# Kernel optimization log

Measured on AMD Instinct MI355X. Metric: run time of the kernel, lower is better.

The kernel has to match this reference:

```python
import jax, jax.numpy as jnp
import numpy as np

PRE_NMS_LIMIT = 6000
PROPOSAL_COUNT = 1000
NMS_THRESHOLD = 0.7
RPN_BBOX_STD_DEV = np.array([0.1, 0.1, 0.2, 0.2], dtype=np.float32)
NEG_INF = -1e30


def setup_inputs() -> dict:
    key = jax.random.key(0)
    k1, k2, k3 = jax.random.split(key, 3)
    B, N = 8, 262144
    rpn_probs = jax.random.uniform(k1, (B, N, 2), dtype=jnp.float32)
    rpn_bbox = jax.random.normal(k2, (B, N, 4), dtype=jnp.float32)
    anchors = jax.random.uniform(k3, (B, N, 4), dtype=jnp.float32)
    return {"rpn_probs": rpn_probs, "rpn_bbox": rpn_bbox, "anchors": anchors}


def apply_box_deltas(boxes, deltas):
    # boxes: [..., (y1,x1,y2,x2)], deltas: [..., (dy,dx,log(dh),log(dw))]
    h = boxes[..., 2] - boxes[..., 0]
    w = boxes[..., 3] - boxes[..., 1]
    cy = boxes[..., 0] + 0.5 * h
    cx = boxes[..., 1] + 0.5 * w
    cy = cy + deltas[..., 0] * h
    cx = cx + deltas[..., 1] * w
    h = h * jnp.exp(deltas[..., 2])
    w = w * jnp.exp(deltas[..., 3])
    y1 = cy - 0.5 * h
    x1 = cx - 0.5 * w
    return jnp.stack([y1, x1, y1 + h, x1 + w], axis=-1)


def clip_boxes(boxes):
    # window = [0, 0, 1, 1]
    return jnp.clip(boxes, 0.0, 1.0)


def nms_single(boxes, scores, max_out, iou_thresh):
    # Greedy NMS on one image. boxes [K,4] (sorted by score desc), scores [K].
    y1, x1, y2, x2 = boxes[:, 0], boxes[:, 1], boxes[:, 2], boxes[:, 3]
    areas = (y2 - y1) * (x2 - x1)

    def step(s, _):
        i = jnp.argmax(s)
        valid = s[i] > NEG_INF
        by1, bx1, by2, bx2 = y1[i], x1[i], y2[i], x2[i]
        iy1 = jnp.maximum(y1, by1)
        ix1 = jnp.maximum(x1, bx1)
        iy2 = jnp.minimum(y2, by2)
        ix2 = jnp.minimum(x2, bx2)
        inter = jnp.maximum(iy2 - iy1, 0.0) * jnp.maximum(ix2 - ix1, 0.0)
        union = areas + areas[i] - inter
        iou = inter / jnp.maximum(union, 1e-12)
        suppress = iou > iou_thresh
        s = jnp.where(suppress, NEG_INF, s)
        s = s.at[i].set(NEG_INF)
        return s, (i, valid)

    s0 = jnp.where(jnp.isfinite(scores), scores, NEG_INF)
    _, (idx, valid) = jax.lax.scan(step, s0, None, length=max_out)
    return idx, valid


def reference(rpn_probs, rpn_bbox, anchors):
    scores = rpn_probs[:, :, 1]                               # [B, N]
    deltas = rpn_bbox * RPN_BBOX_STD_DEV.reshape(1, 1, 4)     # [B, N, 4]

    pre_nms = min(PRE_NMS_LIMIT, anchors.shape[1])
    top_scores, ix = jax.lax.top_k(scores, pre_nms)           # [B, K], [B, K]
    deltas = jnp.take_along_axis(deltas, ix[:, :, None], axis=1)
    pre_nms_anchors = jnp.take_along_axis(anchors, ix[:, :, None], axis=1)

    boxes = clip_boxes(apply_box_deltas(pre_nms_anchors, deltas))  # [B, K, 4]

    idx, valid = jax.vmap(lambda b, s: nms_single(b, s, PROPOSAL_COUNT, NMS_THRESHOLD))(boxes, top_scores)
    sel = jnp.take_along_axis(boxes, idx[:, :, None], axis=1)      # [B, P, 4]
    proposals = jnp.where(valid[:, :, None], sel, 0.0)             # pad invalid with zeros
    return proposals
```

## Files before the change

kernel.cpp:

```cpp
#include <hip/hip_runtime.h>
#include <stdint.h>

#define NB 8
#define NN 262144
#define KTOP 6000
#define CAP 8192
#define NOUT 1000
#define IOU_THR 0.7f
#define NGROUPS ((KTOP + 63) / 64)
#define NF4B (NN * 2 / 4)

#define OFF_HIST 0
#define OFF_CNT  32768
#define OFF_CUT  33792
#define OFF_KEYS 34048
#define OFF_SIDX 558336
#define OFF_CBOX 750336
#define OFF_CAR  1518336

__device__ __forceinline__ int binOf(unsigned int u) {
  if (u & 0x80000000u) return 0;
  if (u >= 0x3F000000u) {
    unsigned int r = 512u + ((u - 0x3F000000u) >> 14);
    return (int)(r > 1023u ? 1023u : r);
  }
  return (int)(u >> 23);
}

__global__ void k0_init(unsigned int* __restrict__ hist, unsigned int* __restrict__ cnt,
                        unsigned long long* __restrict__ keys) {
  int i = blockIdx.x * blockDim.x + threadIdx.x;
  if (i < NB * CAP) keys[i] = ~0ull;
  if (i < NB * 1024) hist[i] = 0u;
  if (i < NB * 32) cnt[i] = 0u;
}

__global__ __launch_bounds__(256) void k1_hist(const float4* __restrict__ probs4,
                                               unsigned int* __restrict__ hist) {
  __shared__ unsigned int lh[1024];
  int t = threadIdx.x;
  for (int i = t; i < 1024; i += 256) lh[i] = 0u;
  __syncthreads();
  int b = blockIdx.x >> 5;
  int blk = blockIdx.x & 31;
  size_t base = (size_t)b * NF4B + (size_t)blk * 4096;
#pragma unroll 4
  for (int it = 0; it < 16; ++it) {
    float4 f = probs4[base + it * 256 + t];
    atomicAdd(&lh[binOf(__float_as_uint(f.y))], 1u);
    atomicAdd(&lh[binOf(__float_as_uint(f.w))], 1u);
  }
  __syncthreads();
  for (int i = t; i < 1024; i += 256)
    if (lh[i]) atomicAdd(&hist[b * 1024 + i], lh[i]);
}

__global__ void k2_cut(const unsigned int* __restrict__ hist, int* __restrict__ cut) {
  int w = threadIdx.x >> 6, lane = threadIdx.x & 63;
  if (w >= NB) return;
  unsigned int carry = 0; int cb = 0; bool found = false;
  for (int c = 0; c < 16 && !found; ++c) {
    int bin = 1023 - c * 64 - lane;
    unsigned int v = hist[w * 1024 + bin];
    unsigned int p = v;
    for (int d = 1; d < 64; d <<= 1) {
      unsigned int q = __shfl_up(p, d);
      if (lane >= d) p += q;
    }
    unsigned int cum = carry + p;
    unsigned long long m = __ballot(cum >= KTOP);
    if (m) { int fl = __builtin_ctzll(m); cb = 1023 - c * 64 - fl; found = true; }
    carry += __shfl(p, 63);
  }
  if (lane == 0) cut[w] = cb;
}

__global__ __launch_bounds__(256) void k3_compact(const float4* __restrict__ probs4,
                                                  const int* __restrict__ cut,
                                                  unsigned int* __restrict__ cnt,
                                                  unsigned long long* __restrict__ keys) {
  __shared__ unsigned int waveSums[4];
  __shared__ unsigned int blockBase;
  int t = threadIdx.x, lane = t & 63, w = t >> 6;
  int b = blockIdx.x >> 5;
  int blk = blockIdx.x & 31;
  int cb = cut[b];
  size_t base = (size_t)b * NF4B + (size_t)blk * 4096;
  unsigned int mask = 0;
#pragma unroll 4
  for (int it = 0; it < 16; ++it) {
    float4 f = probs4[base + it * 256 + t];
    if (binOf(__float_as_uint(f.y)) >= cb) mask |= 1u << (2 * it);
    if (binOf(__float_as_uint(f.w)) >= cb) mask |= 1u << (2 * it + 1);
  }
  unsigned int cntT = __popc(mask);
  unsigned int pre = cntT;
  for (int d = 1; d < 64; d <<= 1) {
    unsigned int q = __shfl_up(pre, d);
    if (lane >= d) pre += q;
  }
  if (lane == 63) waveSums[w] = pre;
  __syncthreads();
  if (t == 0) {
    unsigned int tot = waveSums[0] + waveSums[1] + waveSums[2] + waveSums[3];
    blockBase = atomicAdd(&cnt[b * 32], tot);
  }
  __syncthreads();
  unsigned int mybase = blockBase + (pre - cntT);
  for (int m = 0; m < w; ++m) mybase += waveSums[m];
  if (mask) {
    unsigned int kk = 0;
    for (int it = 0; it < 16; ++it) {
      if (mask & (3u << (2 * it))) {
        float4 f = probs4[base + it * 256 + t];
        unsigned int e0 = ((unsigned int)(blk * 4096 + it * 256 + t)) * 2;
        if (mask & (1u << (2 * it))) {
          unsigned int pos = mybase + kk++;
          if (pos < CAP)
            keys[(size_t)b * CAP + pos] =
                ((unsigned long long)(~__float_as_uint(f.y)) << 32) | e0;
        }
        if (mask & (1u << (2 * it + 1))) {
          unsigned int pos = mybase + kk++;
          if (pos < CAP)
            keys[(size_t)b * CAP + pos] =
                ((unsigned long long)(~__float_as_uint(f.w)) << 32) | (e0 + 1);
        }
      }
    }
  }
}


__global__ __launch_bounds__(128) void k4a_sortchunk(unsigned long long* __restrict__ keys) {
  __shared__ unsigned long long sk[1024];
  int b = blockIdx.x >> 3, c = blockIdx.x & 7;
  int t = threadIdx.x;
  size_t gb = (size_t)b * CAP + (size_t)c * 1024;
  int gl = c * 1024 + 8 * t;
  unsigned long long v[8];
#pragma unroll
  for (int r = 0; r < 8; ++r) v[r] = keys[gb + 8 * t + r];
#pragma unroll
  for (int kk = 2; kk <= 8; kk <<= 1) {
#pragma unroll
    for (int j = kk >> 1; j >= 1; j >>= 1) {
#pragma unroll
      for (int r = 0; r < 8; ++r) {
        if ((r & j) == 0) {
          bool up = (((gl + r) & kk) == 0);
          unsigned long long a = v[r], bb = v[r | j];
          if ((a > bb) == up) { v[r] = bb; v[r | j] = a; }
        }
      }
    }
  }
  for (int kk = 16; kk <= 1024; kk <<= 1) {
    bool up = ((gl & kk) == 0);
    for (int j = kk >> 1; j >= 8; j >>= 1) {
#pragma unroll
      for (int r = 0; r < 8; ++r) sk[r * 128 + t] = v[r];
      __syncthreads();
      int p = t ^ (j >> 3);
      bool lower = ((t & (j >> 3)) == 0);
      bool wmin = (lower == up);
#pragma unroll
      for (int r = 0; r < 8; ++r) {
        unsigned long long pv = sk[r * 128 + p];
        bool gt = v[r] > pv;
        v[r] = (gt == wmin) ? pv : v[r];
      }
      __syncthreads();
    }
#pragma unroll
    for (int j = 4; j >= 1; j >>= 1)
#pragma unroll
      for (int r = 0; r < 8; ++r)
        if ((r & j) == 0) {
          unsigned long long a = v[r], bb = v[r | j];
          if ((a > bb) == up) { v[r] = bb; v[r | j] = a; }
        }
  }
#pragma unroll
  for (int r = 0; r < 8; ++r) keys[gb + 8 * t + r] = v[r];
}

template <int KK>
__global__ __launch_bounds__(KK / 8) void k4_phase(unsigned long long* __restrict__ keys,
                                                   unsigned int* __restrict__ sortedIdx) {
  __shared__ unsigned long long sk[KK];
  constexpr int NT = KK / 8;
  constexpr int NCH = CAP / KK;
  int b = blockIdx.x / NCH, c = blockIdx.x % NCH;
  int t = threadIdx.x;
  size_t gb = (size_t)b * CAP + (size_t)c * KK;
  int gl = c * KK + 8 * t;
  unsigned long long v[8];
#pragma unroll
  for (int r = 0; r < 8; ++r) v[r] = keys[gb + 8 * t + r];
  bool up = ((gl & KK) == 0);
  for (int j = KK >> 1; j >= 8; j >>= 1) {
#pragma unroll
    for (int r = 0; r < 8; ++r) sk[r * NT + t] = v[r];
    __syncthreads();
    int p = t ^ (j >> 3);
    bool lower = ((t & (j >> 3)) == 0);
    bool wmin = (lower == up);
#pragma unroll
    for (int r = 0; r < 8; ++r) {
      unsigned long long pv = sk[r * NT + p];
      bool gt = v[r] > pv;
      v[r] = (gt == wmin) ? pv : v[r];
    }
    __syncthreads();
  }
#pragma unroll
  for (int j = 4; j >= 1; j >>= 1)
#pragma unroll
    for (int r = 0; r < 8; ++r)
      if ((r & j) == 0) {
        unsigned long long a = v[r], bb = v[r | j];
        if ((a > bb) == up) { v[r] = bb; v[r | j] = a; }
      }
  if (KK == CAP) {
#pragma unroll
    for (int r = 0; r < 8; ++r) {
      int gi = gl + r;
      if (gi < KTOP) sortedIdx[b * KTOP + gi] = (unsigned int)(v[r] & 0xFFFFFFFFull);
    }
  } else {
#pragma unroll
    for (int r = 0; r < 8; ++r) keys[gb + 8 * t + r] = v[r];
  }
}

__global__ void k5_boxes(const unsigned int* __restrict__ sortedIdx,
                         const float4* __restrict__ anchors, const float4* __restrict__ bbox,
                         float4* __restrict__ cbox, float* __restrict__ car) {
  int tid = blockIdx.x * blockDim.x + threadIdx.x;
  if (tid >= NB * KTOP) return;
  int b = tid / KTOP;
  unsigned int idx = sortedIdx[tid];
  float4 a = anchors[(size_t)b * NN + idx];
  float4 d = bbox[(size_t)b * NN + idx];
  {
#pragma clang fp contract(off)
    float dy = d.x * 0.1f, dx = d.y * 0.1f, dh = d.z * 0.2f, dw = d.w * 0.2f;
    float h = a.z - a.x;
    float w = a.w - a.y;
    float cy = a.x + 0.5f * h;
    float cx = a.y + 0.5f * w;
    cy = cy + dy * h;
    cx = cx + dx * w;
    h = h * expf(dh);
    w = w * expf(dw);
    float y1 = cy - 0.5f * h;
    float x1 = cx - 0.5f * w;
    float y2 = y1 + h;
    float x2 = x1 + w;
    y1 = fminf(fmaxf(y1, 0.0f), 1.0f);
    x1 = fminf(fmaxf(x1, 0.0f), 1.0f);
    y2 = fminf(fmaxf(y2, 0.0f), 1.0f);
    x2 = fminf(fmaxf(x2, 0.0f), 1.0f);
    float4 o; o.x = y1; o.y = x1; o.z = y2; o.w = x2;
    cbox[tid] = o;
    car[tid] = (y2 - y1) * (x2 - x1);
  }
}

__device__ __forceinline__ bool iouSup(float y1, float x1, float y2, float x2, float ar,
                                       float by1, float bx1, float by2, float bx2, float bar) {
#pragma clang fp contract(off)
  float iy1 = fmaxf(y1, by1);
  float ix1 = fmaxf(x1, bx1);
  float iy2 = fminf(y2, by2);
  float ix2 = fminf(x2, bx2);
  float inter = fmaxf(iy2 - iy1, 0.0f) * fmaxf(ix2 - ix1, 0.0f);
  float uni = (ar + bar) - inter;
  float iou = inter / fmaxf(uni, 1e-12f);
  return iou > IOU_THR;
}

__global__ __launch_bounds__(1024) void k6_nms(const float4* __restrict__ cbox,
                                               const float* __restrict__ car,
                                               float* __restrict__ out) {
  __shared__ float sy1[1088], sx1[1088], sy2[1088], sx2[1088], sar[1088];
  __shared__ float g_y1[2][64], g_x1[2][64], g_y2[2][64], g_x2[2][64], g_ar[2][64];
  __shared__ unsigned long long rowMat[64];
  __shared__ unsigned long long preSuppPart[16];
  __shared__ int nselSh, nsuppSh;
  int b = blockIdx.x, t = threadIdx.x;
  int lane = t & 63, w = t >> 6;

  if (t < 64) {
    if (t < KTOP) {
      float4 bx = cbox[(size_t)b * KTOP + t];
      g_y1[0][t] = bx.x; g_x1[0][t] = bx.y; g_y2[0][t] = bx.z; g_x2[0][t] = bx.w;
      g_ar[0][t] = car[(size_t)b * KTOP + t];
    }
  }
  if (t == 0) { nselSh = 0; nsuppSh = 0; }
  __syncthreads();

  for (int g = 0; g < NGROUPS; ++g) {
    int p = g & 1;
    int gs = g * 64;
    int validCnt = (KTOP - gs < 64) ? (KTOP - gs) : 64;

    if (w == 15 && g + 1 < NGROUPS) {
      int idx2 = gs + 64 + lane;
      if (idx2 < KTOP) {
        float4 bx = cbox[(size_t)b * KTOP + idx2];
        int q = p ^ 1;
        g_y1[q][lane] = bx.x; g_x1[q][lane] = bx.y;
        g_y2[q][lane] = bx.z; g_x2[q][lane] = bx.w;
        g_ar[q][lane] = car[(size_t)b * KTOP + idx2];
      }
    }
    float cy1 = g_y1[p][lane], cx1 = g_x1[p][lane];
    float cy2 = g_y2[p][lane], cx2 = g_x2[p][lane], ca = g_ar[p][lane];
    bool cpos = (cy2 > cy1) && (cx2 > cx1);

    {
      int nsupp = nsuppSh;
      bool s = false;
      if (cpos) {
        for (int si = w; si < nsupp; si += 16) {
          if (iouSup(cy1, cx1, cy2, cx2, ca,
                     sy1[si], sx1[si], sy2[si], sx2[si], sar[si])) { s = true; break; }
        }
      }
      unsigned long long m = __ballot(s);
      if (lane == 0) preSuppPart[w] = m;
    }
#pragma unroll
    for (int r = 0; r < 4; ++r) {
      int i = w * 4 + r;
      float by1 = g_y1[p][i], bx1 = g_x1[p][i];
      float by2 = g_y2[p][i], bx2 = g_x2[p][i], bar = g_ar[p][i];
      unsigned long long rowm = 0ull;
      if ((by2 > by1) && (bx2 > bx1)) {
        bool kill = iouSup(cy1, cx1, cy2, cx2, ca, by1, bx1, by2, bx2, bar);
        rowm = __ballot(kill);
      }
      if (lane == 0) rowMat[i] = rowm;
    }
    __syncthreads();

    if (t < 64) {
      int nsel0 = nselSh, nsupp0 = nsuppSh;
      unsigned long long rr = rowMat[t];
      unsigned int rLo = (unsigned int)rr, rHi = (unsigned int)(rr >> 32);
      unsigned long long preSupp = 0ull;
#pragma unroll
      for (int c2 = 0; c2 < 16; ++c2) preSupp |= preSuppPart[c2];
      unsigned long long validMask =
          (validCnt >= 64) ? ~0ull : ((1ull << validCnt) - 1ull);
      unsigned long long posMask = __ballot(cpos);
      unsigned long long alive = validMask & ~preSupp;
      unsigned long long selm = alive & ~posMask;
      unsigned long long work = alive & posMask;
      while (work) {
        int jj = __builtin_ctzll(work);
        selm |= (1ull << jj);
        unsigned int lo = (unsigned int)__builtin_amdgcn_readlane((int)rLo, jj);
        unsigned int hi = (unsigned int)__builtin_amdgcn_readlane((int)rHi, jj);
        work &= ~(((unsigned long long)hi << 32) | lo);
        work &= ~(1ull << jj);
      }
      bool sel = ((selm >> t) & 1ull) != 0ull;
      if (sel) {
        int rank = nsel0 + (int)__popcll(selm & ((1ull << t) - 1ull));
        if (rank < NOUT) {
          float4 o; o.x = cy1; o.y = cx1; o.z = cy2; o.w = cx2;
          ((float4*)out)[(size_t)b * NOUT + rank] = o;
        }
      }
      bool canSup = sel && cpos;
      unsigned long long csm = __ballot(canSup);
      if (canSup) {
        int rs = nsupp0 + (int)__popcll(csm & ((1ull << t) - 1ull));
        sy1[rs] = cy1; sx1[rs] = cx1; sy2[rs] = cy2; sx2[rs] = cx2; sar[rs] = ca;
      }
      if (t == 0) {
        nselSh = nsel0 + (int)__popcll(selm);
        nsuppSh = nsupp0 + (int)__popcll(csm);
      }
    }
    __syncthreads();
    if (nselSh >= NOUT) break;
  }

  __syncthreads();
  int nf = nselSh < NOUT ? nselSh : NOUT;
  for (int k2 = nf * 4 + t; k2 < NOUT * 4; k2 += 1024)
    out[(size_t)b * NOUT * 4 + k2] = 0.0f;
}

extern "C" void kernel_launch(void* const* d_in, const int* in_sizes, int n_in,
                              void* d_out, int out_size, void* d_ws, size_t ws_size,
                              hipStream_t stream) {
  (void)in_sizes; (void)n_in; (void)out_size; (void)ws_size;
  const float* probs = (const float*)d_in[0];
  const float4* bbox = (const float4*)d_in[1];
  const float4* anchors = (const float4*)d_in[2];
  float* out = (float*)d_out;
  char* ws = (char*)d_ws;

  unsigned int* hist = (unsigned int*)(ws + OFF_HIST);
  unsigned int* cnt = (unsigned int*)(ws + OFF_CNT);
  int* cut = (int*)(ws + OFF_CUT);
  unsigned long long* keys = (unsigned long long*)(ws + OFF_KEYS);
  unsigned int* sidx = (unsigned int*)(ws + OFF_SIDX);
  float4* cbox = (float4*)(ws + OFF_CBOX);
  float* car = (float*)(ws + OFF_CAR);

  k0_init<<<256, 256, 0, stream>>>(hist, cnt, keys);
  k1_hist<<<256, 256, 0, stream>>>((const float4*)probs, hist);
  k2_cut<<<1, 512, 0, stream>>>(hist, cut);
  k3_compact<<<256, 256, 0, stream>>>((const float4*)probs, cut, cnt, keys);
  k4a_sortchunk<<<NB * 8, 128, 0, stream>>>(keys);
  k4_phase<2048><<<NB * 4, 256, 0, stream>>>(keys, sidx);
  k4_phase<4096><<<NB * 2, 512, 0, stream>>>(keys, sidx);
  k4_phase<8192><<<NB, 1024, 0, stream>>>(keys, sidx);
  k5_boxes<<<(NB * KTOP + 255) / 256, 256, 0, stream>>>(sidx, anchors, bbox, cbox, car);
  k6_nms<<<NB, 1024, 0, stream>>>(cbox, car, out);
}
```

Before: 222.7 us.

## Compact positive-area boxes before NMS and emit zero-area selections separately

A scan kernel compacts boxes with positive area into a slot list, so the serial NMS loop iterates only over boxes that can suppress or be suppressed. Zero-area boxes, which are always selected and never suppress, get their output ranks afterwards in an emit kernel using per-group selection bitmasks and prefix counts. NMS also stops early once the remaining zero-area boxes would fill the output. The histogram kernel is simplified to merge low-value bins into a single counter, which reduces shared-memory atomics. This adds two kernel launches and extra workspace traffic.

```diff
diff --git a/kernel.cpp b/kernel.cpp
--- a/kernel.cpp
+++ b/kernel.cpp
@@ -7,8 +7,8 @@
 #define CAP 8192
 #define NOUT 1000
 #define IOU_THR 0.7f
-#define NGROUPS ((KTOP + 63) / 64)
 #define NF4B (NN * 2 / 4)
+#define PPAD 6016
 
 #define OFF_HIST 0
 #define OFF_CNT  32768
@@ -17,14 +17,19 @@
 #define OFF_SIDX 558336
 #define OFF_CBOX 750336
 #define OFF_CAR  1518336
-
-__device__ __forceinline__ int binOf(unsigned int u) {
+#define OFF_NPOS (OFF_HIST + 0)
+#define OFF_SELW (OFF_HIST + 1024)
+#define OFF_SELP (OFF_HIST + 7168)
+#define OFF_STOP (OFF_HIST + 10368)
+#define OFF_NVAL (OFF_HIST + 10624)
+#define OFF_PPRE (OFF_KEYS)
+#define OFF_PSLOT (OFF_KEYS + 192512)
+
+__device__ __forceinline__ int binOf2(unsigned int u) {
   if (u & 0x80000000u) return 0;
-  if (u >= 0x3F000000u) {
-    unsigned int r = 512u + ((u - 0x3F000000u) >> 14);
-    return (int)(r > 1023u ? 1023u : r);
-  }
-  return (int)(u >> 23);
+  if (u < 0x3F000000u) return 0;
+  unsigned int r = (u - 0x3F000000u) >> 14;
+  return (int)(512u + (r > 511u ? 511u : r));
 }
 
 __global__ void k0_init(unsigned int* __restrict__ hist, unsigned int* __restrict__ cnt,
@@ -44,12 +49,17 @@
   int b = blockIdx.x >> 5;
   int blk = blockIdx.x & 31;
   size_t base = (size_t)b * NF4B + (size_t)blk * 4096;
+  unsigned int lowCnt = 0;
 #pragma unroll 4
   for (int it = 0; it < 16; ++it) {
     float4 f = probs4[base + it * 256 + t];
-    atomicAdd(&lh[binOf(__float_as_uint(f.y))], 1u);
-    atomicAdd(&lh[binOf(__float_as_uint(f.w))], 1u);
-  }
+    unsigned int u1 = __float_as_uint(f.y), u2 = __float_as_uint(f.w);
+    if ((u1 & 0x80000000u) || u1 < 0x3F000000u) ++lowCnt;
+    else { unsigned int r = (u1 - 0x3F000000u) >> 14; atomicAdd(&lh[512 + (r > 511u ? 511u : r)], 1u); }
+    if ((u2 & 0x80000000u) || u2 < 0x3F000000u) ++lowCnt;
+    else { unsigned int r = (u2 - 0x3F000000u) >> 14; atomicAdd(&lh[512 + (r > 511u ? 511u : r)], 1u); }
+  }
+  if (lowCnt) atomicAdd(&lh[0], lowCnt);
   __syncthreads();
   for (int i = t; i < 1024; i += 256)
     if (lh[i]) atomicAdd(&hist[b * 1024 + i], lh[i]);
@@ -90,8 +100,8 @@
 #pragma unroll 4
   for (int it = 0; it < 16; ++it) {
     float4 f = probs4[base + it * 256 + t];
-    if (binOf(__float_as_uint(f.y)) >= cb) mask |= 1u << (2 * it);
-    if (binOf(__float_as_uint(f.w)) >= cb) mask |= 1u << (2 * it + 1);
+    if (binOf2(__float_as_uint(f.y)) >= cb) mask |= 1u << (2 * it);
+    if (binOf2(__float_as_uint(f.w)) >= cb) mask |= 1u << (2 * it + 1);
   }
   unsigned int cntT = __popc(mask);
   unsigned int pre = cntT;
@@ -130,7 +140,6 @@
     }
   }
 }
-
 
 __global__ __launch_bounds__(128) void k4a_sortchunk(unsigned long long* __restrict__ keys) {
   __shared__ unsigned long long sk[1024];
@@ -268,6 +277,46 @@
   }
 }
 
+__global__ __launch_bounds__(1024) void k5b_scan(const float4* __restrict__ cbox,
+                                                 unsigned int* __restrict__ posPre,
+                                                 unsigned int* __restrict__ pslot,
+                                                 unsigned int* __restrict__ nposArr) {
+  __shared__ unsigned int waveSums[16];
+  __shared__ unsigned int carrySh;
+  int b = blockIdx.x, t = threadIdx.x, lane = t & 63, w = t >> 6;
+  if (t == 0) carrySh = 0;
+  __syncthreads();
+  for (int base = 0; base < KTOP; base += 1024) {
+    int i = base + t;
+    bool pos = false;
+    if (i < KTOP) {
+      float4 bx = cbox[(size_t)b * KTOP + i];
+      pos = (bx.z > bx.x) && (bx.w > bx.y);
+    }
+    unsigned long long m = __ballot(pos);
+    unsigned int pre = (unsigned int)__popcll(m & ((1ull << lane) - 1ull));
+    if (lane == 0) waveSums[w] = (unsigned int)__popcll(m);
+    __syncthreads();
+    unsigned int wbase = 0, total = 0;
+#pragma unroll
+    for (int mm = 0; mm < 16; ++mm) {
+      unsigned int v = waveSums[mm];
+      if (mm < w) wbase += v;
+      total += v;
+    }
+    unsigned int carry = carrySh;
+    if (i < KTOP) {
+      unsigned int excl = carry + wbase + pre;
+      posPre[(size_t)b * PPAD + i] = excl;
+      if (pos) pslot[(size_t)b * PPAD + excl] = (unsigned int)i;
+    }
+    __syncthreads();
+    if (t == 0) carrySh = carry + total;
+  }
+  __syncthreads();
+  if (t == 0) nposArr[b * 32] = carrySh;
+}
+
 __device__ __forceinline__ bool iouSup(float y1, float x1, float y2, float x2, float ar,
                                        float by1, float bx1, float by2, float bx2, float bar) {
 #pragma clang fp contract(off)
@@ -283,51 +332,53 @@
 
 __global__ __launch_bounds__(1024) void k6_nms(const float4* __restrict__ cbox,
                                                const float* __restrict__ car,
-                                               float* __restrict__ out) {
-  __shared__ float sy1[1088], sx1[1088], sy2[1088], sx2[1088], sar[1088];
-  __shared__ float g_y1[2][64], g_x1[2][64], g_y2[2][64], g_x2[2][64], g_ar[2][64];
+                                               const unsigned int* __restrict__ pslot,
+                                               const unsigned int* __restrict__ nposArr,
+                                               unsigned long long* __restrict__ selW,
+                                               unsigned int* __restrict__ selP,
+                                               unsigned int* __restrict__ stopArr,
+                                               unsigned int* __restrict__ nvalArr) {
+  __shared__ float4 selBox[1088];
+  __shared__ float selAr[1088];
+  __shared__ float4 gbox[2][64];
+  __shared__ float gar[2][64];
   __shared__ unsigned long long rowMat[64];
   __shared__ unsigned long long preSuppPart[16];
-  __shared__ int nselSh, nsuppSh;
-  int b = blockIdx.x, t = threadIdx.x;
-  int lane = t & 63, w = t >> 6;
-
-  if (t < 64) {
-    if (t < KTOP) {
-      float4 bx = cbox[(size_t)b * KTOP + t];
-      g_y1[0][t] = bx.x; g_x1[0][t] = bx.y; g_y2[0][t] = bx.z; g_x2[0][t] = bx.w;
-      g_ar[0][t] = car[(size_t)b * KTOP + t];
-    }
-  }
-  if (t == 0) { nselSh = 0; nsuppSh = 0; }
-  __syncthreads();
-
-  for (int g = 0; g < NGROUPS; ++g) {
-    int p = g & 1;
-    int gs = g * 64;
-    int validCnt = (KTOP - gs < 64) ? (KTOP - gs) : 64;
-
-    if (w == 15 && g + 1 < NGROUPS) {
-      int idx2 = gs + 64 + lane;
-      if (idx2 < KTOP) {
-        float4 bx = cbox[(size_t)b * KTOP + idx2];
+  __shared__ int selCntSh, stopSh;
+  int b = blockIdx.x, t = threadIdx.x, lane = t & 63, w = t >> 6;
+  int npos = (int)nposArr[b * 32];
+  int ngroups = (npos + 63) >> 6;
+  const unsigned int* ps = pslot + (size_t)b * PPAD;
+  if (t == 0) { selCntSh = 0; stopSh = 0; }
+  if (t < 64 && t < npos) {
+    unsigned int s0 = ps[t];
+    gbox[0][t] = cbox[(size_t)b * KTOP + s0];
+    gar[0][t] = car[(size_t)b * KTOP + s0];
+  }
+  __syncthreads();
+
+  for (int g = 0; g < ngroups; ++g) {
+    int p = g & 1, j0 = g * 64;
+    int cnt2 = (npos - j0 < 64) ? (npos - j0) : 64;
+    if (w == 15 && g + 1 < ngroups) {
+      int j2 = j0 + 64 + lane;
+      if (j2 < npos) {
+        unsigned int s2 = ps[j2];
         int q = p ^ 1;
-        g_y1[q][lane] = bx.x; g_x1[q][lane] = bx.y;
-        g_y2[q][lane] = bx.z; g_x2[q][lane] = bx.w;
-        g_ar[q][lane] = car[(size_t)b * KTOP + idx2];
-      }
-    }
-    float cy1 = g_y1[p][lane], cx1 = g_x1[p][lane];
-    float cy2 = g_y2[p][lane], cx2 = g_x2[p][lane], ca = g_ar[p][lane];
-    bool cpos = (cy2 > cy1) && (cx2 > cx1);
-
+        gbox[q][lane] = cbox[(size_t)b * KTOP + s2];
+        gar[q][lane] = car[(size_t)b * KTOP + s2];
+      }
+    }
+    float4 cb4 = gbox[p][lane];
+    float ca = gar[p][lane];
     {
-      int nsupp = nsuppSh;
+      int nsel = selCntSh;
       bool s = false;
-      if (cpos) {
-        for (int si = w; si < nsupp; si += 16) {
-          if (iouSup(cy1, cx1, cy2, cx2, ca,
-                     sy1[si], sx1[si], sy2[si], sx2[si], sar[si])) { s = true; break; }
+      if (lane < cnt2) {
+        for (int si = w; si < nsel; si += 16) {
+          float4 sb = selBox[si];
+          if (iouSup(cb4.x, cb4.y, cb4.z, cb4.w, ca,
+                     sb.x, sb.y, sb.z, sb.w, selAr[si])) { s = true; break; }
         }
       }
       unsigned long long m = __ballot(s);
@@ -336,30 +387,27 @@
 #pragma unroll
     for (int r = 0; r < 4; ++r) {
       int i = w * 4 + r;
-      float by1 = g_y1[p][i], bx1 = g_x1[p][i];
-      float by2 = g_y2[p][i], bx2 = g_x2[p][i], bar = g_ar[p][i];
       unsigned long long rowm = 0ull;
-      if ((by2 > by1) && (bx2 > bx1)) {
-        bool kill = iouSup(cy1, cx1, cy2, cx2, ca, by1, bx1, by2, bx2, bar);
+      if (i < cnt2) {
+        float4 rb = gbox[p][i];
+        float rar = gar[p][i];
+        bool kill = (lane < cnt2) &&
+                    iouSup(cb4.x, cb4.y, cb4.z, cb4.w, ca, rb.x, rb.y, rb.z, rb.w, rar);
         rowm = __ballot(kill);
       }
       if (lane == 0) rowMat[i] = rowm;
     }
     __syncthreads();
-
     if (t < 64) {
-      int nsel0 = nselSh, nsupp0 = nsuppSh;
+      int nsel0 = selCntSh;
       unsigned long long rr = rowMat[t];
       unsigned int rLo = (unsigned int)rr, rHi = (unsigned int)(rr >> 32);
-      unsigned long long preSupp = 0ull;
-#pragma unroll
-      for (int c2 = 0; c2 < 16; ++c2) preSupp |= preSuppPart[c2];
-      unsigned long long validMask =
-          (validCnt >= 64) ? ~0ull : ((1ull << validCnt) - 1ull);
-      unsigned long long posMask = __ballot(cpos);
-      unsigned long long alive = validMask & ~preSupp;
-      unsigned long long selm = alive & ~posMask;
-      unsigned long long work = alive & posMask;
+      unsigned long long pre = 0ull;
+#pragma unroll
+      for (int c2 = 0; c2 < 16; ++c2) pre |= preSuppPart[c2];
+      unsigned long long validMask = (cnt2 >= 64) ? ~0ull : ((1ull << cnt2) - 1ull);
+      unsigned long long work = validMask & ~pre;
+      unsigned long long selm = 0ull;
       while (work) {
         int jj = __builtin_ctzll(work);
         selm |= (1ull << jj);
@@ -370,30 +418,72 @@
       }
       bool sel = ((selm >> t) & 1ull) != 0ull;
       if (sel) {
-        int rank = nsel0 + (int)__popcll(selm & ((1ull << t) - 1ull));
-        if (rank < NOUT) {
-          float4 o; o.x = cy1; o.y = cx1; o.z = cy2; o.w = cx2;
-          ((float4*)out)[(size_t)b * NOUT + rank] = o;
-        }
-      }
-      bool canSup = sel && cpos;
-      unsigned long long csm = __ballot(canSup);
-      if (canSup) {
-        int rs = nsupp0 + (int)__popcll(csm & ((1ull << t) - 1ull));
-        sy1[rs] = cy1; sx1[rs] = cx1; sy2[rs] = cy2; sx2[rs] = cx2; sar[rs] = ca;
+        int rs = nsel0 + (int)__popcll(selm & ((1ull << t) - 1ull));
+        selBox[rs] = cb4;
+        selAr[rs] = ca;
       }
       if (t == 0) {
-        nselSh = nsel0 + (int)__popcll(selm);
-        nsuppSh = nsupp0 + (int)__popcll(csm);
+        int nsNew = nsel0 + (int)__popcll(selm);
+        selW[b * 96 + g] = selm;
+        selP[b * 100 + g] = (unsigned int)nsel0;
+        selCntSh = nsNew;
+        int j0n = j0 + 64;
+        int stop = 0;
+        unsigned int stopSlot = KTOP;
+        if (nsNew >= NOUT) {
+          stop = 1;
+          if (j0n < npos) stopSlot = ps[j0n];
+        } else if (j0n < npos) {
+          unsigned int nslot = ps[j0n];
+          if ((int)(nslot - (unsigned int)j0n) + nsNew >= NOUT) { stop = 1; stopSlot = nslot; }
+        }
+        if (stop) {
+          stopSh = 1;
+          selP[b * 100 + g + 1] = (unsigned int)nsNew;
+          stopArr[b * 8] = stopSlot;
+          nvalArr[b * 8] = NOUT;
+        } else if (j0n >= npos) {
+          selP[b * 100 + g + 1] = (unsigned int)nsNew;
+          stopArr[b * 8] = KTOP;
+          int T = (KTOP - npos) + nsNew;
+          nvalArr[b * 8] = (unsigned int)(T < NOUT ? T : NOUT);
+        }
       }
     }
     __syncthreads();
-    if (nselSh >= NOUT) break;
-  }
-
-  __syncthreads();
-  int nf = nselSh < NOUT ? nselSh : NOUT;
-  for (int k2 = nf * 4 + t; k2 < NOUT * 4; k2 += 1024)
+    if (stopSh) break;
+  }
+  if (ngroups == 0 && t == 0) {
+    selP[b * 100] = 0;
+    stopArr[b * 8] = KTOP;
+    nvalArr[b * 8] = (KTOP < NOUT ? KTOP : NOUT);
+  }
+}
+
+__global__ __launch_bounds__(1024) void k7_emit(const float4* __restrict__ cbox,
+                                                const unsigned int* __restrict__ posPre,
+                                                const unsigned long long* __restrict__ selW,
+                                                const unsigned int* __restrict__ selP,
+                                                const unsigned int* __restrict__ stopArr,
+                                                const unsigned int* __restrict__ nvalArr,
+                                                float* __restrict__ out) {
+  int b = blockIdx.x, t = threadIdx.x;
+  unsigned int stopSlot = stopArr[b * 8];
+  for (int i = t; i < KTOP; i += 1024) {
+    if ((unsigned int)i >= stopSlot) continue;
+    float4 bx = cbox[(size_t)b * KTOP + i];
+    bool pos = (bx.z > bx.x) && (bx.w > bx.y);
+    unsigned int pp = posPre[(size_t)b * PPAD + i];
+    unsigned long long word = selW[b * 96 + (pp >> 6)];
+    unsigned int selBefore = selP[b * 100 + (pp >> 6)] +
+                             (unsigned int)__popcll(word & ((1ull << (pp & 63)) - 1ull));
+    bool chosen = pos ? (((word >> (pp & 63)) & 1ull) != 0ull) : true;
+    if (!chosen) continue;
+    unsigned int rank = ((unsigned int)i - pp) + selBefore;
+    if (rank < NOUT) ((float4*)out)[(size_t)b * NOUT + rank] = bx;
+  }
+  unsigned int nval = nvalArr[b * 8];
+  for (int k2 = (int)nval * 4 + t; k2 < NOUT * 4; k2 += 1024)
     out[(size_t)b * NOUT * 4 + k2] = 0.0f;
 }
 
@@ -414,6 +504,13 @@
   unsigned int* sidx = (unsigned int*)(ws + OFF_SIDX);
   float4* cbox = (float4*)(ws + OFF_CBOX);
   float* car = (float*)(ws + OFF_CAR);
+  unsigned int* posPre = (unsigned int*)(ws + OFF_PPRE);
+  unsigned int* pslot = (unsigned int*)(ws + OFF_PSLOT);
+  unsigned int* nposArr = (unsigned int*)(ws + OFF_NPOS);
+  unsigned long long* selW = (unsigned long long*)(ws + OFF_SELW);
+  unsigned int* selP = (unsigned int*)(ws + OFF_SELP);
+  unsigned int* stopArr = (unsigned int*)(ws + OFF_STOP);
+  unsigned int* nvalArr = (unsigned int*)(ws + OFF_NVAL);
 
   k0_init<<<256, 256, 0, stream>>>(hist, cnt, keys);
   k1_hist<<<256, 256, 0, stream>>>((const float4*)probs, hist);
@@ -424,5 +521,7 @@
   k4_phase<4096><<<NB * 2, 512, 0, stream>>>(keys, sidx);
   k4_phase<8192><<<NB, 1024, 0, stream>>>(keys, sidx);
   k5_boxes<<<(NB * KTOP + 255) / 256, 256, 0, stream>>>(sidx, anchors, bbox, cbox, car);
-  k6_nms<<<NB, 1024, 0, stream>>>(cbox, car, out);
-}
+  k5b_scan<<<NB, 1024, 0, stream>>>(cbox, posPre, pslot, nposArr);
+  k6_nms<<<NB, 1024, 0, stream>>>(cbox, car, pslot, nposArr, selW, selP, stopArr, nvalArr);
+  k7_emit<<<NB, 1024, 0, stream>>>(cbox, posPre, selW, selP, stopArr, nvalArr, out);
+}
```

New measurement: 207.2 us. -6.9%, faster.
